# Kernel tuning notes

Measured on AMD Instinct MI355X. Metric: run time of the kernel, lower is better.

The kernel has to match this reference:

```python
import jax, jax.numpy as jnp
import numpy as np

T, B, N_IN, N_OUT = 100, 32, 1024, 512
LR_LTP, LR_LTD = 1e-4, -1e-4
TAU_PRE, TAU_POST, DT = 20.0, 20.0, 1.0
W_MIN, W_MAX = 0.0, 1.0
SPIKE_PROB = 0.05


def setup_inputs() -> dict:
    key = jax.random.key(0)
    k1, k2, k3 = jax.random.split(key, 3)
    weight = jax.random.uniform(k1, (N_OUT, N_IN), dtype=jnp.float32)
    pre_spikes = (jax.random.uniform(k2, (T, B, N_IN)) < SPIKE_PROB).astype(jnp.float32)
    post_spikes = (jax.random.uniform(k3, (T, B, N_OUT)) < SPIKE_PROB).astype(jnp.float32)
    pre_trace = jnp.zeros((B, N_IN), jnp.float32)
    post_trace = jnp.zeros((B, N_OUT), jnp.float32)
    return {"weight": weight, "pre_spikes": pre_spikes, "post_spikes": post_spikes,
            "pre_trace": pre_trace, "post_trace": post_trace}


def reference(weight, pre_spikes, post_spikes, pre_trace, post_trace):
    # weight: [N_out, N_in]; pre_spikes: [T,B,N_in]; post_spikes: [T,B,N_out]
    decay_pre = jnp.exp(jnp.asarray(-DT / TAU_PRE, weight.dtype))
    decay_post = jnp.exp(jnp.asarray(-DT / TAU_POST, weight.dtype))
    # Soft bounds (w_max=1.0 > 0 -> w_max - w; w_min=0.0 not < 0 -> w)
    soft_ltp = W_MAX - weight
    soft_ltd = weight
    Bf = jnp.asarray(pre_spikes.shape[1], weight.dtype)

    def step(carry, xs):
        pre_tr, post_tr, dw = carry
        pre_s, post_s = xs  # [B,N_in], [B,N_out]
        pre_tr = pre_tr * decay_pre + pre_s
        post_tr = post_tr * decay_post + post_s
        # batch-mean of outer products -> [N_out, N_in]
        ltp_mean = jnp.einsum('bo,bi->oi', post_s, pre_tr) / Bf
        ltd_mean = jnp.einsum('bo,bi->oi', post_tr, pre_s) / Bf
        dw = dw + LR_LTP * soft_ltp * ltp_mean + LR_LTD * soft_ltd * ltd_mean
        return (pre_tr, post_tr, dw), None

    init = (pre_trace, post_trace, jnp.zeros_like(weight))
    (pre_tr, post_tr, delta_w), _ = jax.lax.scan(step, init, (pre_spikes, post_spikes))
    return delta_w, pre_tr, post_tr
```

## Files before the change

### kernel.cpp

```cpp
#include <hip/hip_runtime.h>

typedef unsigned short ushort;
typedef unsigned int uint;
typedef unsigned char uchar;
typedef __attribute__((ext_vector_type(8))) int intx8;
typedef __attribute__((ext_vector_type(16))) float floatx16;

#define T_STEPS 100
#define BATCH   32
#define NIN     1024
#define NOUT    512

#define SEG      112
#define KPAD     (BATCH * SEG)
#define KSTRIDEB 3648
#define KS       8
#define KCHUNK   (KPAD / KS)

#define LR_LTP  (1e-4f)
#define LR_LTD  (-1e-4f)
#define INV_B   (1.0f / 32.0f)
#define DECAY   0.951229424500714f
#define D28     0.246596963941607f
#define TCH     28
#define NCHUNK  4

#define OFF_PRE  (NOUT * NIN)
#define OFF_POST (OFF_PRE + BATCH * NIN)

#define B_PRST  0
#define B_PRTT  ((size_t)NIN * KSTRIDEB)
#define B_POST  ((size_t)2 * NIN * KSTRIDEB)
#define B_POTT  ((size_t)2 * NIN * KSTRIDEB + (size_t)NOUT * KSTRIDEB)
#define B_END   ((size_t)2 * (NIN + NOUT) * KSTRIDEB)
#define SLABU   (NOUT * NIN + 128)


static __device__ __forceinline__ uint pk4_fp8(float a, float b, float c, float d) {
    uint v = 0;
    v = __builtin_amdgcn_cvt_pk_fp8_f32(a, b, v, false);
    v = __builtin_amdgcn_cvt_pk_fp8_f32(c, d, v, true);
    return v;
}

static __device__ __forceinline__ ushort f2bf(float f) {
    union { float f; unsigned int u; } v; v.f = f;
    unsigned int r = (v.u + 0x7FFFu + ((v.u >> 16) & 1u)) >> 16;
    return (ushort)r;
}

__global__ __launch_bounds__(256) void stdp_traces_t(
    const float* __restrict__ pre_s,
    const float* __restrict__ post_s,
    const float* __restrict__ pre_tr0,
    const float* __restrict__ post_tr0,
    uchar* __restrict__ pre_s_t, uchar* __restrict__ pre_tr_t,
    uchar* __restrict__ post_s_t, uchar* __restrict__ post_tr_t,
    float* __restrict__ out)
{
    __shared__ uint Ls[64 * 33];
    __shared__ uint Lt[64 * 33];
    __shared__ float Eend[NCHUNK][64];

    const int chain = threadIdx.x & 63;
    const int c     = threadIdx.x >> 6;
    const int g     = blockIdx.x * 64 + chain;

    const float* src; const float* init;
    int id, stride, outoff;
    if (g < BATCH * NIN) {
        src = pre_s;  init = pre_tr0;
        id = g;               stride = BATCH * NIN;  outoff = OFF_PRE;
    } else {
        src = post_s; init = post_tr0;
        id = g - BATCH * NIN; stride = BATCH * NOUT; outoff = OFF_POST;
    }

    const int t0 = c * TCH;
    float x[TCH];
    #pragma unroll
    for (int m = 0; m < TCH; ++m)
        x[m] = (t0 + m < T_STEPS) ? src[(size_t)(t0 + m) * stride + id] : 0.f;

    uint sp[7];
    #pragma unroll
    for (int j = 0; j < 7; ++j)
        sp[j] = pk4_fp8(x[4*j], x[4*j+1], x[4*j+2], x[4*j+3]);

    float e = 0.f;
    #pragma unroll
    for (int m = 0; m < TCH; ++m) { e = e * DECAY + x[m]; x[m] = e; }
    Eend[c][chain] = e;
    __syncthreads();

    float C = init[id];
    for (int cc = 0; cc < c; ++cc) C = C * D28 + Eend[cc][chain];
    float p = C * DECAY;
    #pragma unroll
    for (int m = 0; m < TCH; ++m) { x[m] += p; p *= DECAY; }

    if (c == NCHUNK - 1) out[outoff + id] = x[15];

    #pragma unroll
    for (int j = 0; j < 7; ++j) {
        const uint tj = pk4_fp8(x[4*j], x[4*j+1], x[4*j+2], x[4*j+3]);
        Ls[chain * 33 + c * 7 + j] = sp[j];
        Lt[chain * 33 + c * 7 + j] = tj;
    }
    __syncthreads();

    const int id0 = blockIdx.x * 64;
    uchar *dS, *dT; int b0, ch0;
    if (id0 < BATCH * NIN) {
        b0 = id0 >> 10; ch0 = id0 & 1023; dS = pre_s_t;  dT = pre_tr_t;
    } else {
        const int idq = id0 - BATCH * NIN;
        b0 = idq >> 9;  ch0 = idq & 511;  dS = post_s_t; dT = post_tr_t;
    }
    #pragma unroll
    for (int j = 0; j < 4; ++j) {
        const int q = threadIdx.x + 256 * j;
        if (q < 896) {
            const int op = q >= 448;
            const int qq = q - op * 448;
            const int r  = qq / 7;
            const int cc = qq - r * 7;
            const uint* l = (op ? Lt : Ls) + r * 33 + cc * 4;
            const uint4 v = make_uint4(l[0], l[1], l[2], l[3]);
            uchar* gd = (op ? dT : dS) + (size_t)(ch0 + r) * KSTRIDEB + b0 * SEG + cc * 16;
            *(uint4*)gd = v;
        }
    }
}

static __device__ __forceinline__ intx8 ld32(const uchar* p) {
    const uint4 lo = *(const uint4*)p;
    const uint4 hv = *(const uint4*)(p + 16);
    intx8 r;
    r[0] = (int)lo.x; r[1] = (int)lo.y; r[2] = (int)lo.z; r[3] = (int)lo.w;
    r[4] = (int)hv.x; r[5] = (int)hv.y; r[6] = (int)hv.z; r[7] = (int)hv.w;
    return r;
}

__global__ __launch_bounds__(256, 2) void stdp_gemm_dual(
    const uchar* __restrict__ post_s_t, const uchar* __restrict__ pre_tr_t,
    const uchar* __restrict__ post_tr_t, const uchar* __restrict__ pre_s_t,
    const float* __restrict__ wmat, ushort* __restrict__ Spart)
{
    const int kz = blockIdx.x;
    const int i0 = blockIdx.y * 64;
    const int o0 = blockIdx.z * 128;
    const int k0 = kz * KCHUNK;

    const int tid  = threadIdx.x;
    const int w    = tid >> 6;
    const int lane = tid & 63;
    const int wm   = w & 1;
    const int wn   = w >> 1;
    const int l32  = lane & 31;
    const int hi   = lane >> 5;

    floatx16 accP[2], accD[2];
    #pragma unroll
    for (int mt = 0; mt < 2; ++mt)
        #pragma unroll
        for (int r = 0; r < 16; ++r) { accP[mt][r] = 0.f; accD[mt][r] = 0.f; }

    const size_t aBase = (size_t)(o0 + wm * 64 + l32) * KSTRIDEB;
    const size_t bBase = (size_t)(i0 + wn * 32 + l32) * KSTRIDEB;

    for (int kb = k0; kb < k0 + KCHUNK; kb += 64) {
        const int ko = kb + (hi << 5);
        intx8 aP[2], aD[2], bP, bD;
        #pragma unroll
        for (int mt = 0; mt < 2; ++mt) {
            const size_t off = aBase + (size_t)(mt * 32) * KSTRIDEB + ko;
            aP[mt] = ld32(post_s_t  + off);
            aD[mt] = ld32(post_tr_t + off);
        }
        {
            const size_t off = bBase + ko;
            bP = ld32(pre_tr_t + off);
            bD = ld32(pre_s_t  + off);
        }
        #pragma unroll
        for (int mt = 0; mt < 2; ++mt) {
            accP[mt] = __builtin_amdgcn_mfma_scale_f32_32x32x64_f8f6f4(
                aP[mt], bP, accP[mt], 0, 0, 0, 127, 0, 127);
            accD[mt] = __builtin_amdgcn_mfma_scale_f32_32x32x64_f8f6f4(
                aD[mt], bD, accD[mt], 0, 0, 0, 127, 0, 127);
        }
    }

    ushort* Sz = Spart + (size_t)kz * SLABU;
    const float c1 = LR_LTP * INV_B;
    const float c2 = LR_LTD * INV_B;
    #pragma unroll
    for (int mt = 0; mt < 2; ++mt) {
        const int ob = o0 + wm * 64 + mt * 32 + hi * 4;
        const int i  = i0 + wn * 32 + l32;
        #pragma unroll
        for (int r = 0; r < 16; ++r) {
            const int o = ob + (r & 3) + 8 * (r >> 2);
            const size_t idx = (size_t)o * NIN + i;
            const float wv = wmat[idx];
            const float v = c1 * (1.0f - wv) * accP[mt][r]
                          + c2 * wv          * accD[mt][r];
            Sz[idx] = f2bf(v);
        }
    }
}

__global__ __launch_bounds__(128) void stdp_finalize(
    const ushort* __restrict__ Spart, float* __restrict__ out)
{
    const int j = blockIdx.x * blockDim.x + threadIdx.x;
    float s[8] = {0.f, 0.f, 0.f, 0.f, 0.f, 0.f, 0.f, 0.f};
    #pragma unroll
    for (int z = 0; z < KS; ++z) {
        const uint4 v = *(const uint4*)(Spart + (size_t)z * SLABU + (size_t)j * 8);
        const uint u[4] = {v.x, v.y, v.z, v.w};
        #pragma unroll
        for (int q = 0; q < 4; ++q) {
            union { uint u; float f; } lo, hi;
            lo.u = u[q] << 16;
            hi.u = u[q] & 0xFFFF0000u;
            s[2 * q]     += lo.f;
            s[2 * q + 1] += hi.f;
        }
    }
    float4* o = (float4*)(out + (size_t)j * 8);
    o[0] = make_float4(s[0], s[1], s[2], s[3]);
    o[1] = make_float4(s[4], s[5], s[6], s[7]);
}

extern "C" void kernel_launch(void* const* d_in, const int* in_sizes, int n_in,
                              void* d_out, int out_size, void* d_ws, size_t ws_size,
                              hipStream_t stream) {
    const float* weight   = (const float*)d_in[0];
    const float* pre_s    = (const float*)d_in[1];
    const float* post_s   = (const float*)d_in[2];
    const float* pre_tr0  = (const float*)d_in[3];
    const float* post_tr0 = (const float*)d_in[4];
    float* out = (float*)d_out;

    uchar* wsb = (uchar*)d_ws;
    uchar* pre_s_t   = wsb + B_PRST;
    uchar* pre_tr_t  = wsb + B_PRTT;
    uchar* post_s_t  = wsb + B_POST;
    uchar* post_tr_t = wsb + B_POTT;
    ushort* Spart    = (ushort*)(wsb + B_END);

    stdp_traces_t<<<dim3(BATCH * (NIN + NOUT) / 64), dim3(256), 0, stream>>>(
        pre_s, post_s, pre_tr0, post_tr0,
        pre_s_t, pre_tr_t, post_s_t, post_tr_t, out);

    stdp_gemm_dual<<<dim3(KS, NIN / 64, NOUT / 128), dim3(256), 0, stream>>>(
        post_s_t, pre_tr_t, post_tr_t, pre_s_t, weight, Spart);

    stdp_finalize<<<dim3((NOUT * NIN / 8) / 128), dim3(128), 0, stream>>>(
        Spart, out);
}
```

Before: 98.41 us.

## Fuse trace, GEMM and reduction kernels into one cooperative kernel with grid syncs

```diff
diff --git a/kernel.cpp b/kernel.cpp
--- a/kernel.cpp
+++ b/kernel.cpp
@@ -1,4 +1,7 @@
 #include <hip/hip_runtime.h>
+#include <hip/hip_cooperative_groups.h>
+
+namespace cg = cooperative_groups;
 
 typedef unsigned short ushort;
 typedef unsigned int uint;
@@ -35,6 +38,8 @@
 #define B_END   ((size_t)2 * (NIN + NOUT) * KSTRIDEB)
 #define SLABU   (NOUT * NIN + 128)
 
+#define GRID    512
+
 
 static __device__ __forceinline__ uint pk4_fp8(float a, float b, float c, float d) {
     uint v = 0;
@@ -49,22 +54,26 @@
     return (ushort)r;
 }
 
-__global__ __launch_bounds__(256) void stdp_traces_t(
-    const float* __restrict__ pre_s,
-    const float* __restrict__ post_s,
-    const float* __restrict__ pre_tr0,
-    const float* __restrict__ post_tr0,
+static __device__ __forceinline__ intx8 ld32(const uchar* p) {
+    const uint4 lo = *(const uint4*)p;
+    const uint4 hv = *(const uint4*)(p + 16);
+    intx8 r;
+    r[0] = (int)lo.x; r[1] = (int)lo.y; r[2] = (int)lo.z; r[3] = (int)lo.w;
+    r[4] = (int)hv.x; r[5] = (int)hv.y; r[6] = (int)hv.z; r[7] = (int)hv.w;
+    return r;
+}
+
+static __device__ __forceinline__ void phaseA(
+    int vbid, uint* Ls, uint* Lt, float (*Eend)[64],
+    const float* __restrict__ pre_s, const float* __restrict__ post_s,
+    const float* __restrict__ pre_tr0, const float* __restrict__ post_tr0,
     uchar* __restrict__ pre_s_t, uchar* __restrict__ pre_tr_t,
     uchar* __restrict__ post_s_t, uchar* __restrict__ post_tr_t,
     float* __restrict__ out)
 {
-    __shared__ uint Ls[64 * 33];
-    __shared__ uint Lt[64 * 33];
-    __shared__ float Eend[NCHUNK][64];
-
     const int chain = threadIdx.x & 63;
     const int c     = threadIdx.x >> 6;
-    const int g     = blockIdx.x * 64 + chain;
+    const int g     = vbid * 64 + chain;
 
     const float* src; const float* init;
     int id, stride, outoff;
@@ -109,7 +118,7 @@
     }
     __syncthreads();
 
-    const int id0 = blockIdx.x * 64;
+    const int id0 = vbid * 64;
     uchar *dS, *dT; int b0, ch0;
     if (id0 < BATCH * NIN) {
         b0 = id0 >> 10; ch0 = id0 & 1023; dS = pre_s_t;  dT = pre_tr_t;
@@ -133,105 +142,114 @@
     }
 }
 
-static __device__ __forceinline__ intx8 ld32(const uchar* p) {
-    const uint4 lo = *(const uint4*)p;
-    const uint4 hv = *(const uint4*)(p + 16);
-    intx8 r;
-    r[0] = (int)lo.x; r[1] = (int)lo.y; r[2] = (int)lo.z; r[3] = (int)lo.w;
-    r[4] = (int)hv.x; r[5] = (int)hv.y; r[6] = (int)hv.z; r[7] = (int)hv.w;
-    return r;
-}
-
-__global__ __launch_bounds__(256, 2) void stdp_gemm_dual(
-    const uchar* __restrict__ post_s_t, const uchar* __restrict__ pre_tr_t,
-    const uchar* __restrict__ post_tr_t, const uchar* __restrict__ pre_s_t,
-    const float* __restrict__ wmat, ushort* __restrict__ Spart)
+__global__ __launch_bounds__(256, 2) void stdp_fused(
+    const float* __restrict__ pre_s, const float* __restrict__ post_s,
+    const float* __restrict__ pre_tr0, const float* __restrict__ post_tr0,
+    const float* __restrict__ wmat,
+    uchar* __restrict__ pre_s_t, uchar* __restrict__ pre_tr_t,
+    uchar* __restrict__ post_s_t, uchar* __restrict__ post_tr_t,
+    ushort* __restrict__ Spart, float* __restrict__ out)
 {
-    const int kz = blockIdx.x;
-    const int i0 = blockIdx.y * 64;
-    const int o0 = blockIdx.z * 128;
-    const int k0 = kz * KCHUNK;
-
-    const int tid  = threadIdx.x;
-    const int w    = tid >> 6;
-    const int lane = tid & 63;
-    const int wm   = w & 1;
-    const int wn   = w >> 1;
-    const int l32  = lane & 31;
-    const int hi   = lane >> 5;
-
-    floatx16 accP[2], accD[2];
-    #pragma unroll
-    for (int mt = 0; mt < 2; ++mt)
+    __shared__ uint Ls[64 * 33];
+    __shared__ uint Lt[64 * 33];
+    __shared__ float Eend[NCHUNK][64];
+
+    phaseA(blockIdx.x, Ls, Lt, Eend, pre_s, post_s, pre_tr0, post_tr0,
+           pre_s_t, pre_tr_t, post_s_t, post_tr_t, out);
+    if (blockIdx.x < 256)
+        phaseA(blockIdx.x + GRID, Ls, Lt, Eend, pre_s, post_s, pre_tr0, post_tr0,
+               pre_s_t, pre_tr_t, post_s_t, post_tr_t, out);
+
+    cg::this_grid().sync();
+
+    {
+        const int bid = blockIdx.x;
+        const int kz = bid & 7;
+        const int iy = (bid >> 3) & 15;
+        const int oz = bid >> 7;
+        const int i0 = iy * 64;
+        const int o0 = oz * 128;
+        const int k0 = kz * KCHUNK;
+
+        const int tid  = threadIdx.x;
+        const int w    = tid >> 6;
+        const int lane = tid & 63;
+        const int wm   = w & 1;
+        const int wn   = w >> 1;
+        const int l32  = lane & 31;
+        const int hi   = lane >> 5;
+
+        floatx16 accP[2], accD[2];
         #pragma unroll
-        for (int r = 0; r < 16; ++r) { accP[mt][r] = 0.f; accD[mt][r] = 0.f; }
-
-    const size_t aBase = (size_t)(o0 + wm * 64 + l32) * KSTRIDEB;
-    const size_t bBase = (size_t)(i0 + wn * 32 + l32) * KSTRIDEB;
-
-    for (int kb = k0; kb < k0 + KCHUNK; kb += 64) {
-        const int ko = kb + (hi << 5);
-        intx8 aP[2], aD[2], bP, bD;
+        for (int mt = 0; mt < 2; ++mt)
+            #pragma unroll
+            for (int r = 0; r < 16; ++r) { accP[mt][r] = 0.f; accD[mt][r] = 0.f; }
+
+        const size_t aBase = (size_t)(o0 + wm * 64 + l32) * KSTRIDEB;
+        const size_t bBase = (size_t)(i0 + wn * 32 + l32) * KSTRIDEB;
+
+        for (int kb = k0; kb < k0 + KCHUNK; kb += 64) {
+            const int ko = kb + (hi << 5);
+            intx8 aP[2], aD[2], bP, bD;
+            #pragma unroll
+            for (int mt = 0; mt < 2; ++mt) {
+                const size_t off = aBase + (size_t)(mt * 32) * KSTRIDEB + ko;
+                aP[mt] = ld32(post_s_t  + off);
+                aD[mt] = ld32(post_tr_t + off);
+            }
+            {
+                const size_t off = bBase + ko;
+                bP = ld32(pre_tr_t + off);
+                bD = ld32(pre_s_t  + off);
+            }
+            #pragma unroll
+            for (int mt = 0; mt < 2; ++mt) {
+                accP[mt] = __builtin_amdgcn_mfma_scale_f32_32x32x64_f8f6f4(
+                    aP[mt], bP, accP[mt], 0, 0, 0, 127, 0, 127);
+                accD[mt] = __builtin_amdgcn_mfma_scale_f32_32x32x64_f8f6f4(
+                    aD[mt], bD, accD[mt], 0, 0, 0, 127, 0, 127);
+            }
+        }
+
+        ushort* Sz = Spart + (size_t)kz * SLABU;
+        const float c1 = LR_LTP * INV_B;
+        const float c2 = LR_LTD * INV_B;
         #pragma unroll
         for (int mt = 0; mt < 2; ++mt) {
-            const size_t off = aBase + (size_t)(mt * 32) * KSTRIDEB + ko;
-            aP[mt] = ld32(post_s_t  + off);
-            aD[mt] = ld32(post_tr_t + off);
-        }
-        {
-            const size_t off = bBase + ko;
-            bP = ld32(pre_tr_t + off);
-            bD = ld32(pre_s_t  + off);
-        }
+            const int ob = o0 + wm * 64 + mt * 32 + hi * 4;
+            const int i  = i0 + wn * 32 + l32;
+            #pragma unroll
+            for (int r = 0; r < 16; ++r) {
+                const int o = ob + (r & 3) + 8 * (r >> 2);
+                const size_t idx = (size_t)o * NIN + i;
+                const float wv = wmat[idx];
+                const float v = c1 * (1.0f - wv) * accP[mt][r]
+                              + c2 * wv          * accD[mt][r];
+                Sz[idx] = f2bf(v);
+            }
+        }
+    }
+
+    cg::this_grid().sync();
+
+    {
+        const int j4 = blockIdx.x * 256 + threadIdx.x;
+        float s[4] = {0.f, 0.f, 0.f, 0.f};
         #pragma unroll
-        for (int mt = 0; mt < 2; ++mt) {
-            accP[mt] = __builtin_amdgcn_mfma_scale_f32_32x32x64_f8f6f4(
-                aP[mt], bP, accP[mt], 0, 0, 0, 127, 0, 127);
-            accD[mt] = __builtin_amdgcn_mfma_scale_f32_32x32x64_f8f6f4(
-                aD[mt], bD, accD[mt], 0, 0, 0, 127, 0, 127);
-        }
-    }
-
-    ushort* Sz = Spart + (size_t)kz * SLABU;
-    const float c1 = LR_LTP * INV_B;
-    const float c2 = LR_LTD * INV_B;
-    #pragma unroll
-    for (int mt = 0; mt < 2; ++mt) {
-        const int ob = o0 + wm * 64 + mt * 32 + hi * 4;
-        const int i  = i0 + wn * 32 + l32;
-        #pragma unroll
-        for (int r = 0; r < 16; ++r) {
-            const int o = ob + (r & 3) + 8 * (r >> 2);
-            const size_t idx = (size_t)o * NIN + i;
-            const float wv = wmat[idx];
-            const float v = c1 * (1.0f - wv) * accP[mt][r]
-                          + c2 * wv          * accD[mt][r];
-            Sz[idx] = f2bf(v);
-        }
-    }
-}
-
-__global__ __launch_bounds__(128) void stdp_finalize(
-    const ushort* __restrict__ Spart, float* __restrict__ out)
-{
-    const int j = blockIdx.x * blockDim.x + threadIdx.x;
-    float s[8] = {0.f, 0.f, 0.f, 0.f, 0.f, 0.f, 0.f, 0.f};
-    #pragma unroll
-    for (int z = 0; z < KS; ++z) {
-        const uint4 v = *(const uint4*)(Spart + (size_t)z * SLABU + (size_t)j * 8);
-        const uint u[4] = {v.x, v.y, v.z, v.w};
-        #pragma unroll
-        for (int q = 0; q < 4; ++q) {
-            union { uint u; float f; } lo, hi;
-            lo.u = u[q] << 16;
-            hi.u = u[q] & 0xFFFF0000u;
-            s[2 * q]     += lo.f;
-            s[2 * q + 1] += hi.f;
-        }
-    }
-    float4* o = (float4*)(out + (size_t)j * 8);
-    o[0] = make_float4(s[0], s[1], s[2], s[3]);
-    o[1] = make_float4(s[4], s[5], s[6], s[7]);
+        for (int z = 0; z < KS; ++z) {
+            const uint2 v = *(const uint2*)(Spart + (size_t)z * SLABU + (size_t)j4 * 4);
+            const uint u[2] = {v.x, v.y};
+            #pragma unroll
+            for (int q = 0; q < 2; ++q) {
+                union { uint u; float f; } lo, hi;
+                lo.u = u[q] << 16;
+                hi.u = u[q] & 0xFFFF0000u;
+                s[2 * q]     += lo.f;
+                s[2 * q + 1] += hi.f;
+            }
+        }
+        *(float4*)(out + (size_t)j4 * 4) = make_float4(s[0], s[1], s[2], s[3]);
+    }
 }
 
 extern "C" void kernel_launch(void* const* d_in, const int* in_sizes, int n_in,
@@ -251,13 +269,12 @@
     uchar* post_tr_t = wsb + B_POTT;
     ushort* Spart    = (ushort*)(wsb + B_END);
 
-    stdp_traces_t<<<dim3(BATCH * (NIN + NOUT) / 64), dim3(256), 0, stream>>>(
-        pre_s, post_s, pre_tr0, post_tr0,
-        pre_s_t, pre_tr_t, post_s_t, post_tr_t, out);
-
-    stdp_gemm_dual<<<dim3(KS, NIN / 64, NOUT / 128), dim3(256), 0, stream>>>(
-        post_s_t, pre_tr_t, post_tr_t, pre_s_t, weight, Spart);
-
-    stdp_finalize<<<dim3((NOUT * NIN / 8) / 128), dim3(128), 0, stream>>>(
-        Spart, out);
-}
+    void* args[] = {
+        (void*)&pre_s, (void*)&post_s, (void*)&pre_tr0, (void*)&post_tr0,
+        (void*)&weight,
+        (void*)&pre_s_t, (void*)&pre_tr_t, (void*)&post_s_t, (void*)&post_tr_t,
+        (void*)&Spart, (void*)&out
+    };
+    hipLaunchCooperativeKernel((const void*)stdp_fused, dim3(GRID), dim3(256),
+                               args, 0, stream);
+}
```

Result: slower. 244.8 us (+148.7%).

## Drop split-K and finalize kernel; compute full K per smaller output tile

Applied to the files above, without the earlier changes.

```diff
diff --git a/kernel.cpp b/kernel.cpp
--- a/kernel.cpp
+++ b/kernel.cpp
@@ -14,8 +14,6 @@
 #define SEG      112
 #define KPAD     (BATCH * SEG)
 #define KSTRIDEB 3648
-#define KS       8
-#define KCHUNK   (KPAD / KS)
 
 #define LR_LTP  (1e-4f)
 #define LR_LTD  (-1e-4f)
@@ -32,8 +30,6 @@
 #define B_PRTT  ((size_t)NIN * KSTRIDEB)
 #define B_POST  ((size_t)2 * NIN * KSTRIDEB)
 #define B_POTT  ((size_t)2 * NIN * KSTRIDEB + (size_t)NOUT * KSTRIDEB)
-#define B_END   ((size_t)2 * (NIN + NOUT) * KSTRIDEB)
-#define SLABU   (NOUT * NIN + 128)
 
 
 static __device__ __forceinline__ uint pk4_fp8(float a, float b, float c, float d) {
@@ -43,10 +39,13 @@
     return v;
 }
 
-static __device__ __forceinline__ ushort f2bf(float f) {
-    union { float f; unsigned int u; } v; v.f = f;
-    unsigned int r = (v.u + 0x7FFFu + ((v.u >> 16) & 1u)) >> 16;
-    return (ushort)r;
+static __device__ __forceinline__ intx8 ld32(const uchar* p) {
+    const uint4 lo = *(const uint4*)p;
+    const uint4 hv = *(const uint4*)(p + 16);
+    intx8 r;
+    r[0] = (int)lo.x; r[1] = (int)lo.y; r[2] = (int)lo.z; r[3] = (int)lo.w;
+    r[4] = (int)hv.x; r[5] = (int)hv.y; r[6] = (int)hv.z; r[7] = (int)hv.w;
+    return r;
 }
 
 __global__ __launch_bounds__(256) void stdp_traces_t(
@@ -133,105 +132,49 @@
     }
 }
 
-static __device__ __forceinline__ intx8 ld32(const uchar* p) {
-    const uint4 lo = *(const uint4*)p;
-    const uint4 hv = *(const uint4*)(p + 16);
-    intx8 r;
-    r[0] = (int)lo.x; r[1] = (int)lo.y; r[2] = (int)lo.z; r[3] = (int)lo.w;
-    r[4] = (int)hv.x; r[5] = (int)hv.y; r[6] = (int)hv.z; r[7] = (int)hv.w;
-    return r;
-}
-
-__global__ __launch_bounds__(256, 2) void stdp_gemm_dual(
+__global__ __launch_bounds__(128) void stdp_gemm_dual(
     const uchar* __restrict__ post_s_t, const uchar* __restrict__ pre_tr_t,
     const uchar* __restrict__ post_tr_t, const uchar* __restrict__ pre_s_t,
-    const float* __restrict__ wmat, ushort* __restrict__ Spart)
+    const float* __restrict__ wmat, float* __restrict__ out)
 {
-    const int kz = blockIdx.x;
-    const int i0 = blockIdx.y * 64;
-    const int o0 = blockIdx.z * 128;
-    const int k0 = kz * KCHUNK;
+    const int i0 = blockIdx.x * 64;
+    const int o0 = blockIdx.y * 32;
 
     const int tid  = threadIdx.x;
-    const int w    = tid >> 6;
+    const int wn   = tid >> 6;
     const int lane = tid & 63;
-    const int wm   = w & 1;
-    const int wn   = w >> 1;
     const int l32  = lane & 31;
     const int hi   = lane >> 5;
 
-    floatx16 accP[2], accD[2];
-    #pragma unroll
-    for (int mt = 0; mt < 2; ++mt)
-        #pragma unroll
-        for (int r = 0; r < 16; ++r) { accP[mt][r] = 0.f; accD[mt][r] = 0.f; }
-
-    const size_t aBase = (size_t)(o0 + wm * 64 + l32) * KSTRIDEB;
-    const size_t bBase = (size_t)(i0 + wn * 32 + l32) * KSTRIDEB;
-
-    for (int kb = k0; kb < k0 + KCHUNK; kb += 64) {
-        const int ko = kb + (hi << 5);
-        intx8 aP[2], aD[2], bP, bD;
-        #pragma unroll
-        for (int mt = 0; mt < 2; ++mt) {
-            const size_t off = aBase + (size_t)(mt * 32) * KSTRIDEB + ko;
-            aP[mt] = ld32(post_s_t  + off);
-            aD[mt] = ld32(post_tr_t + off);
-        }
-        {
-            const size_t off = bBase + ko;
-            bP = ld32(pre_tr_t + off);
-            bD = ld32(pre_s_t  + off);
-        }
-        #pragma unroll
-        for (int mt = 0; mt < 2; ++mt) {
-            accP[mt] = __builtin_amdgcn_mfma_scale_f32_32x32x64_f8f6f4(
-                aP[mt], bP, accP[mt], 0, 0, 0, 127, 0, 127);
-            accD[mt] = __builtin_amdgcn_mfma_scale_f32_32x32x64_f8f6f4(
-                aD[mt], bD, accD[mt], 0, 0, 0, 127, 0, 127);
-        }
-    }
-
-    ushort* Sz = Spart + (size_t)kz * SLABU;
+    floatx16 accP, accD;
+    #pragma unroll
+    for (int r = 0; r < 16; ++r) { accP[r] = 0.f; accD[r] = 0.f; }
+
+    const size_t aBase = (size_t)(o0 + l32) * KSTRIDEB + (hi << 5);
+    const size_t bBase = (size_t)(i0 + wn * 32 + l32) * KSTRIDEB + (hi << 5);
+
+    for (int kb = 0; kb < KPAD; kb += 64) {
+        const intx8 aP = ld32(post_s_t  + aBase + kb);
+        const intx8 aD = ld32(post_tr_t + aBase + kb);
+        const intx8 bP = ld32(pre_tr_t  + bBase + kb);
+        const intx8 bD = ld32(pre_s_t   + bBase + kb);
+        accP = __builtin_amdgcn_mfma_scale_f32_32x32x64_f8f6f4(
+            aP, bP, accP, 0, 0, 0, 127, 0, 127);
+        accD = __builtin_amdgcn_mfma_scale_f32_32x32x64_f8f6f4(
+            aD, bD, accD, 0, 0, 0, 127, 0, 127);
+    }
+
     const float c1 = LR_LTP * INV_B;
     const float c2 = LR_LTD * INV_B;
-    #pragma unroll
-    for (int mt = 0; mt < 2; ++mt) {
-        const int ob = o0 + wm * 64 + mt * 32 + hi * 4;
-        const int i  = i0 + wn * 32 + l32;
-        #pragma unroll
-        for (int r = 0; r < 16; ++r) {
-            const int o = ob + (r & 3) + 8 * (r >> 2);
-            const size_t idx = (size_t)o * NIN + i;
-            const float wv = wmat[idx];
-            const float v = c1 * (1.0f - wv) * accP[mt][r]
-                          + c2 * wv          * accD[mt][r];
-            Sz[idx] = f2bf(v);
-        }
-    }
-}
-
-__global__ __launch_bounds__(128) void stdp_finalize(
-    const ushort* __restrict__ Spart, float* __restrict__ out)
-{
-    const int j = blockIdx.x * blockDim.x + threadIdx.x;
-    float s[8] = {0.f, 0.f, 0.f, 0.f, 0.f, 0.f, 0.f, 0.f};
-    #pragma unroll
-    for (int z = 0; z < KS; ++z) {
-        const uint4 v = *(const uint4*)(Spart + (size_t)z * SLABU + (size_t)j * 8);
-        const uint u[4] = {v.x, v.y, v.z, v.w};
-        #pragma unroll
-        for (int q = 0; q < 4; ++q) {
-            union { uint u; float f; } lo, hi;
-            lo.u = u[q] << 16;
-            hi.u = u[q] & 0xFFFF0000u;
-            s[2 * q]     += lo.f;
-            s[2 * q + 1] += hi.f;
-        }
-    }
-    float4* o = (float4*)(out + (size_t)j * 8);
-    o[0] = make_float4(s[0], s[1], s[2], s[3]);
-    o[1] = make_float4(s[4], s[5], s[6], s[7]);
+    const int i  = i0 + wn * 32 + l32;
+    const int ob = o0 + hi * 4;
+    #pragma unroll
+    for (int r = 0; r < 16; ++r) {
+        const int o = ob + (r & 3) + 8 * (r >> 2);
+        const size_t idx = (size_t)o * NIN + i;
+        const float wv = wmat[idx];
+        out[idx] = c1 * (1.0f - wv) * accP[r] + c2 * wv * accD[r];
+    }
 }
 
 extern "C" void kernel_launch(void* const* d_in, const int* in_sizes, int n_in,
@@ -249,15 +192,11 @@
     uchar* pre_tr_t  = wsb + B_PRTT;
     uchar* post_s_t  = wsb + B_POST;
     uchar* post_tr_t = wsb + B_POTT;
-    ushort* Spart    = (ushort*)(wsb + B_END);
 
     stdp_traces_t<<<dim3(BATCH * (NIN + NOUT) / 64), dim3(256), 0, stream>>>(
         pre_s, post_s, pre_tr0, post_tr0,
         pre_s_t, pre_tr_t, post_s_t, post_tr_t, out);
 
-    stdp_gemm_dual<<<dim3(KS, NIN / 64, NOUT / 128), dim3(256), 0, stream>>>(
-        post_s_t, pre_tr_t, post_tr_t, pre_s_t, weight, Spart);
-
-    stdp_finalize<<<dim3((NOUT * NIN / 8) / 128), dim3(128), 0, stream>>>(
-        Spart, out);
-}
+    stdp_gemm_dual<<<dim3(NIN / 64, NOUT / 32), dim3(128), 0, stream>>>(
+        post_s_t, pre_tr_t, post_tr_t, pre_s_t, weight, out);
+}
```

New measurement: 104.4 us. +6.0%, slower.
